# Performance work log

Hardware: AMD Instinct MI355X
Metric: run time of the kernel (lower is better)

The kernel has to match this reference:

```python
import jax, jax.numpy as jnp
import numpy as np


def _knn_idx(query, ref, k):
    # query [B,Q,F], ref [B,M,F] -> indices [B,Q,k] of k nearest refs (L2)
    d2 = (jnp.sum(query * query, -1)[..., None]
          - 2.0 * jnp.einsum('bqf,bmf->bqm', query, ref)
          + jnp.sum(ref * ref, -1)[:, None, :])
    _, idx = jax.lax.top_k(-d2, k)
    return idx


def _gather(pts, idx):
    # pts [B,M,F], idx [B,Q,k] -> [B,Q,k,F]
    return jax.vmap(lambda p, i: p[i])(pts, idx)


def _mlp(h, W1, b1, W2, b2):
    # pointwise 1x1-conv MLP: Conv1d(k=1) == per-point matmul
    return jax.nn.relu(h @ W1 + b1) @ W2 + b2


def setup_inputs() -> dict:
    key = jax.random.key(0)
    ks = jax.random.split(key, 12)
    B, N, S1, S2 = 8, 16384, 512, 128

    def p(k, shape, fan):
        return jax.random.normal(k, shape, jnp.float32) / np.float32(np.sqrt(fan))

    return {
        'x': jax.random.normal(ks[0], (B, N, 3), jnp.float32),
        'sample_idx1': jnp.sort(jax.random.randint(ks[1], (S1,), 0, N)),
        'sample_idx2': jnp.sort(jax.random.randint(ks[2], (S2,), 0, S1)),
        'sa1_W1': p(ks[3], (3, 64), 3), 'sa1_b1': jnp.zeros((64,), jnp.float32),
        'sa1_W2': p(ks[4], (64, 64), 64), 'sa1_b2': jnp.zeros((64,), jnp.float32),
        'sa2_W1': p(ks[5], (64, 128), 64), 'sa2_b1': jnp.zeros((128,), jnp.float32),
        'sa2_W2': p(ks[6], (128, 128), 128), 'sa2_b2': jnp.zeros((128,), jnp.float32),
        'fp1_W1': p(ks[7], (192, 64), 192), 'fp1_b1': jnp.zeros((64,), jnp.float32),
        'fp1_W2': p(ks[8], (64, 64), 64), 'fp1_b2': jnp.zeros((64,), jnp.float32),
        'fp2_W1': p(ks[9], (67, 32), 67), 'fp2_b1': jnp.zeros((32,), jnp.float32),
        'fp2_W2': p(ks[10], (32, 32), 32), 'fp2_b2': jnp.zeros((32,), jnp.float32),
        'fc_W': p(ks[11], (32, 2), 32), 'fc_b': jnp.zeros((2,), jnp.float32),
    }


def reference(x, sample_idx1, sample_idx2,
              sa1_W1, sa1_b1, sa1_W2, sa1_b2,
              sa2_W1, sa2_b1, sa2_W2, sa2_b2,
              fp1_W1, fp1_b1, fp1_W2, fp1_b2,
              fp2_W1, fp2_b1, fp2_W2, fp2_b2,
              fc_W, fc_b):
    G = 32  # group_points
    # --- SetAbstraction 1 (KNN grouping in xyz space) ---
    samp1 = x[:, sample_idx1]                                  # [B,S1,3]
    g1 = _gather(x, _knn_idx(samp1, x, G))                     # [B,S1,G,3]
    feat1 = jnp.max(_mlp(g1, sa1_W1, sa1_b1, sa1_W2, sa1_b2), axis=2)   # [B,S1,64]
    # --- SetAbstraction 2 (point cloud = SA1 features, as in source) ---
    samp2 = feat1[:, sample_idx2]                              # [B,S2,64]
    g2 = _gather(feat1, _knn_idx(samp2, feat1, G))             # [B,S2,G,64]
    feat2 = jnp.max(_mlp(g2, sa2_W1, sa2_b1, sa2_W2, sa2_b2), axis=2)   # [B,S2,128]
    coords2 = samp1[:, sample_idx2]                            # [B,S2,3]
    # --- FeaturePropagation 1: interpolate feat2 onto the S1 points (3-NN mean) ---
    interp1 = jnp.mean(_gather(feat2, _knn_idx(samp1, coords2, 3)), axis=2)  # [B,S1,128]
    h1 = _mlp(jnp.concatenate([feat1, interp1], -1), fp1_W1, fp1_b1, fp1_W2, fp1_b2)  # [B,S1,64]
    # --- FeaturePropagation 2: interpolate onto all N points ---
    interp2 = jnp.mean(_gather(h1, _knn_idx(x, samp1, 3)), axis=2)           # [B,N,64]
    h2 = _mlp(jnp.concatenate([x, interp2], -1), fp2_W1, fp2_b1, fp2_W2, fp2_b2)      # [B,N,32]
    return jax.nn.sigmoid(h2 @ fc_W + fc_b)                    # [B,N,2]
```

## Files before the change

### kernel.cpp

```cpp
#include <hip/hip_runtime.h>
#include <hip/hip_bf16.h>

#define NB   8
#define NPTS 16384
#define NS1  512
#define NS2  128
#define KNN  32
#define FINF 3.402823466e+38f

__device__ __forceinline__ unsigned sortkey(float f) {
  unsigned u = __float_as_uint(f);
  unsigned m = (u & 0x80000000u) ? 0xFFFFFFFFu : 0x80000000u;
  return u ^ m;
}

__device__ __forceinline__ void topk32_round(unsigned long long key, int lane,
                                             unsigned long long& lkey,
                                             unsigned long long& tau) {
  unsigned long long mask = __ballot(key < tau);
  while (mask) {
    int src = __ffsll(mask) - 1;
    mask &= mask - 1;
    unsigned long long cand = __shfl(key, src);
    if (cand < tau) {
      unsigned long long up = __shfl_up(lkey, 1);
      if (lane == 0) up = 0ull;
      unsigned long long nk = (lkey < cand) ? lkey : (up < cand ? cand : up);
      if (lane < 32) lkey = nk;
      tau = __shfl(lkey, 31);
    }
  }
}

__device__ __forceinline__ void merge3(float& d0, int& j0, float& d1, int& j1,
                                       float& d2, int& j2, int xm) {
  float e0 = __shfl_xor(d0, xm), e1 = __shfl_xor(d1, xm), e2 = __shfl_xor(d2, xm);
  int   f0 = __shfl_xor(j0, xm), f1 = __shfl_xor(j1, xm), f2 = __shfl_xor(j2, xm);
  float a0 = d0, a1 = d1, a2 = d2;
  int   b0 = j0, b1 = j1, b2 = j2;
  float od0, od1, od2; int oj0, oj1, oj2;
  #pragma unroll
  for (int r = 0; r < 3; ++r) {
    bool ta = (a0 < e0) || (a0 == e0 && b0 < f0);
    float sd = ta ? a0 : e0; int sj = ta ? b0 : f0;
    a0 = ta ? a1 : a0;  b0 = ta ? b1 : b0;
    a1 = ta ? a2 : a1;  b1 = ta ? b2 : b1;
    a2 = ta ? FINF : a2;
    e0 = ta ? e0 : e1;  f0 = ta ? f0 : f1;
    e1 = ta ? e1 : e2;  f1 = ta ? f1 : f2;
    e2 = ta ? e2 : FINF;
    if (r == 0) { od0 = sd; oj0 = sj; }
    else if (r == 1) { od1 = sd; oj1 = sj; }
    else { od2 = sd; oj2 = sj; }
  }
  d0 = od0; j0 = oj0; d1 = od1; j1 = oj1; d2 = od2; j2 = oj2;
}

extern "C" __global__ void __launch_bounds__(256)
prep_kernel(const float* __restrict__ x, float4* __restrict__ xr) {
  const int i = blockIdx.x * 256 + threadIdx.x;
  const float rx = x[i*3+0], ry = x[i*3+1], rz = x[i*3+2];
  xr[i] = make_float4(rx, ry, rz, rx*rx + ry*ry + rz*rz);
}

extern "C" __global__ void __launch_bounds__(256)
knn1_kernel(const float4* __restrict__ xr, const int* __restrict__ sidx1,
            int* __restrict__ idx1) {
  const int w = threadIdx.x >> 6, lane = threadIdx.x & 63;
  const int gq = blockIdx.x * 4 + w;
  const int b = gq >> 9, q = gq & (NS1 - 1);
  const float4* xb = xr + (size_t)b * NPTS;
  const float4 Q = xb[sidx1[q]];
  unsigned long long lkey = ~0ull, tau = ~0ull;
  float4 r = xb[lane];
  for (int t = 0; t < NPTS/64; ++t) {
    float4 rn = r;
    if (t < NPTS/64 - 1) rn = xb[(t+1)*64 + lane];
    const float d = (Q.w - 2.0f*(Q.x*r.x + Q.y*r.y + Q.z*r.z)) + r.w;
    const unsigned long long key =
        ((unsigned long long)sortkey(d) << 32) | (unsigned)(t*64 + lane);
    unsigned long long mask = __ballot(key < tau);
    while (mask) {
      const int src = (int)(__ffsll((long long)mask) - 1);
      mask &= mask - 1;
      const unsigned clo = (unsigned)__builtin_amdgcn_readlane((int)(unsigned)key, src);
      const unsigned chi = (unsigned)__builtin_amdgcn_readlane((int)(unsigned)(key >> 32), src);
      const unsigned long long cand = ((unsigned long long)chi << 32) | clo;
      if (cand < tau) {
        unsigned long long up = __shfl_up(lkey, 1);
        if (lane == 0) up = 0ull;
        unsigned long long nk = (lkey < cand) ? lkey : (up < cand ? cand : up);
        if (lane < 32) lkey = nk;
        const unsigned tlo = (unsigned)__builtin_amdgcn_readlane((int)(unsigned)lkey, 31);
        const unsigned thi = (unsigned)__builtin_amdgcn_readlane((int)(unsigned)(lkey >> 32), 31);
        tau = ((unsigned long long)thi << 32) | tlo;
      }
    }
    r = rn;
  }
  if (lane < 32) idx1[gq*KNN + lane] = (int)(unsigned)lkey;
}

extern "C" __global__ void __launch_bounds__(256)
mlp1_kernel(const float* __restrict__ x, const int* __restrict__ sidx1,
            const int* __restrict__ idx1,
            const float* __restrict__ W1, const float* __restrict__ b1,
            const float* __restrict__ W2, const float* __restrict__ b2,
            float* __restrict__ feat1, float* __restrict__ rr1,
            float* __restrict__ samp1) {
  __shared__ float P[32][3];
  __shared__ float H[32][64];
  __shared__ float PM[4][64];
  const int tid = threadIdx.x;
  const int gq = blockIdx.x;
  const int b = gq >> 9, q = gq & (NS1-1);
  const float* xb = x + (size_t)b * NPTS * 3;
  const int* nb = idx1 + gq * KNN;
  if (tid < 96) { int n = tid/3, d = tid - n*3; P[n][d] = xb[nb[n]*3 + d]; }
  __syncthreads();
  #pragma unroll
  for (int i = 0; i < 8; ++i) {
    int e = tid + 256*i, n = e >> 6, c = e & 63;
    float h = b1[c] + P[n][0]*W1[c] + P[n][1]*W1[64+c] + P[n][2]*W1[128+c];
    H[n][c] = fmaxf(h, 0.0f);
  }
  __syncthreads();
  const int g = tid >> 6, c = tid & 63;
  float acc[8];
  #pragma unroll
  for (int k = 0; k < 8; ++k) acc[k] = 0.0f;
  for (int j = 0; j < 64; j += 4) {
    float w0 = W2[j*64+c], w1 = W2[(j+1)*64+c], w2 = W2[(j+2)*64+c], w3 = W2[(j+3)*64+c];
    #pragma unroll
    for (int k = 0; k < 8; ++k) {
      float4 h4 = *(const float4*)&H[g*8+k][j];
      acc[k] = fmaf(h4.w, w3, fmaf(h4.z, w2, fmaf(h4.y, w1, fmaf(h4.x, w0, acc[k]))));
    }
  }
  float m = acc[0];
  #pragma unroll
  for (int k = 1; k < 8; ++k) m = fmaxf(m, acc[k]);
  PM[g][c] = m;
  __syncthreads();
  if (tid < 64) {
    float v = fmaxf(fmaxf(PM[0][tid], PM[1][tid]), fmaxf(PM[2][tid], PM[3][tid])) + b2[tid];
    feat1[(size_t)gq*64 + tid] = v;
    float s = v*v;
    #pragma unroll
    for (int off = 32; off; off >>= 1) s += __shfl_xor(s, off);
    if (tid == 0) rr1[gq] = s;
  } else if (tid < 67) {
    int d = tid - 64;
    samp1[(size_t)gq*3 + d] = xb[sidx1[q]*3 + d];
  }
}

extern "C" __global__ void __launch_bounds__(256)
knn2_kernel(const float* __restrict__ feat1, const float* __restrict__ rr1,
            const int* __restrict__ sidx2, int* __restrict__ idx2) {
  __shared__ float qrow[4][64];
  const int w = threadIdx.x >> 6, lane = threadIdx.x & 63;
  const int gq = blockIdx.x*4 + w;
  const int b = gq >> 7, q = gq & (NS2-1);
  const int sq = sidx2[q];
  const float* f1b = feat1 + (size_t)b * NS1 * 64;
  const float* rrb = rr1 + b * NS1;
  qrow[w][lane] = f1b[sq*64 + lane];
  __syncthreads();
  const float qq = rrb[sq];
  unsigned long long lkey = ~0ull, tau = ~0ull;
  for (int t = 0; t < NS1/64; ++t) {
    const int j = t*64 + lane;
    const float* rrow = f1b + j*64;
    float dot = 0.0f;
    #pragma unroll
    for (int f = 0; f < 64; f += 4) {
      float4 r4 = *(const float4*)(rrow + f);
      dot = fmaf(qrow[w][f+3], r4.w, fmaf(qrow[w][f+2], r4.z,
            fmaf(qrow[w][f+1], r4.y, fmaf(qrow[w][f+0], r4.x, dot))));
    }
    const float d = (qq - 2.0f*dot) + rrb[j];
    const unsigned long long key =
        ((unsigned long long)sortkey(d) << 32) | (unsigned)j;
    topk32_round(key, lane, lkey, tau);
  }
  if (lane < 32) idx2[gq*KNN + lane] = (int)(unsigned)lkey;
}

extern "C" __global__ void __launch_bounds__(256)
mlp2_kernel(const float* __restrict__ feat1, const int* __restrict__ idx2,
            const float* __restrict__ W1, const float* __restrict__ b1,
            const float* __restrict__ W2, const float* __restrict__ b2,
            float* __restrict__ feat2) {
  __shared__ float Gm[32][64];
  __shared__ float H[32][128];
  __shared__ float PM[2][128];
  const int tid = threadIdx.x;
  const int gq = blockIdx.x;
  const int b = gq >> 7;
  const float* f1b = feat1 + (size_t)b * NS1 * 64;
  const int* nb = idx2 + gq * KNN;
  #pragma unroll
  for (int i = 0; i < 8; ++i) {
    int e = tid + 256*i, n = e >> 6, f = e & 63;
    Gm[n][f] = f1b[nb[n]*64 + f];
  }
  __syncthreads();
  #pragma unroll
  for (int i = 0; i < 16; ++i) {
    int e = tid + 256*i, n = e >> 7, c = e & 127;
    float h = b1[c];
    for (int f = 0; f < 64; f += 4) {
      float4 g4 = *(const float4*)&Gm[n][f];
      h = fmaf(g4.x, W1[f*128+c], h);
      h = fmaf(g4.y, W1[(f+1)*128+c], h);
      h = fmaf(g4.z, W1[(f+2)*128+c], h);
      h = fmaf(g4.w, W1[(f+3)*128+c], h);
    }
    H[n][c] = fmaxf(h, 0.0f);
  }
  __syncthreads();
  const int g = tid >> 7, c = tid & 127;
  float acc[16];
  #pragma unroll
  for (int k = 0; k < 16; ++k) acc[k] = 0.0f;
  for (int j = 0; j < 128; j += 4) {
    float w0 = W2[j*128+c], w1 = W2[(j+1)*128+c], w2 = W2[(j+2)*128+c], w3 = W2[(j+3)*128+c];
    #pragma unroll
    for (int k = 0; k < 16; ++k) {
      float4 h4 = *(const float4*)&H[g*16+k][j];
      acc[k] = fmaf(h4.w, w3, fmaf(h4.z, w2, fmaf(h4.y, w1, fmaf(h4.x, w0, acc[k]))));
    }
  }
  float m = acc[0];
  #pragma unroll
  for (int k = 1; k < 16; ++k) m = fmaxf(m, acc[k]);
  PM[g][c] = m;
  __syncthreads();
  if (tid < 128) feat2[(size_t)gq*128 + tid] = fmaxf(PM[0][tid], PM[1][tid]) + b2[tid];
}

extern "C" __global__ void __launch_bounds__(256)
fp1_kernel(const float* __restrict__ samp1, const int* __restrict__ sidx2,
           const float* __restrict__ feat1, const float* __restrict__ feat2,
           const float* __restrict__ W1, const float* __restrict__ b1,
           const float* __restrict__ W2, const float* __restrict__ b2,
           float* __restrict__ h1) {
  __shared__ float interp[4][128];
  __shared__ float hbuf[4][64];
  const int w = threadIdx.x >> 6, lane = threadIdx.x & 63;
  const int gq = blockIdx.x*4 + w;
  const int b = gq >> 9, q = gq & (NS1-1);
  const float* s1b = samp1 + (size_t)b * NS1 * 3;
  const float qx = s1b[q*3+0], qy = s1b[q*3+1], qz = s1b[q*3+2];
  const float qq = qx*qx + qy*qy + qz*qz;
  float d0, d1; int j0i, j1i;
  {
    const int rs = sidx2[lane];
    const float rx = s1b[rs*3+0], ry = s1b[rs*3+1], rz = s1b[rs*3+2];
    d0 = (qq - 2.0f*(qx*rx+qy*ry+qz*rz)) + (rx*rx+ry*ry+rz*rz);
    j0i = lane;
  }
  {
    const int j = lane + 64;
    const int rs = sidx2[j];
    const float rx = s1b[rs*3+0], ry = s1b[rs*3+1], rz = s1b[rs*3+2];
    d1 = (qq - 2.0f*(qx*rx+qy*ry+qz*rz)) + (rx*rx+ry*ry+rz*rz);
    j1i = j;
  }
  if (d1 < d0) { float td = d0; d0 = d1; d1 = td; int tj = j0i; j0i = j1i; j1i = tj; }
  float dA = d0, dB = d1, dC = FINF;
  int   jA = j0i, jB = j1i, jC = 0;
  merge3(dA, jA, dB, jB, dC, jC, 1);
  merge3(dA, jA, dB, jB, dC, jC, 2);
  merge3(dA, jA, dB, jB, dC, jC, 4);
  merge3(dA, jA, dB, jB, dC, jC, 8);
  merge3(dA, jA, dB, jB, dC, jC, 16);
  merge3(dA, jA, dB, jB, dC, jC, 32);
  const int r0 = jA, r1 = jB, r2 = jC;
  const float* f2b = feat2 + (size_t)b * NS2 * 128;
  interp[w][lane] =
      (f2b[r0*128+lane] + f2b[r1*128+lane] + f2b[r2*128+lane]) * (1.0f/3.0f);
  interp[w][lane+64] =
      (f2b[r0*128+64+lane] + f2b[r1*128+64+lane] + f2b[r2*128+64+lane]) * (1.0f/3.0f);
  __syncthreads();
  const float* f1row = feat1 + (size_t)gq * 64;
  float h = b1[lane];
  for (int f = 0; f < 64; ++f)  h = fmaf(f1row[f], W1[f*64+lane], h);
  for (int f = 0; f < 128; ++f) h = fmaf(interp[w][f], W1[(64+f)*64+lane], h);
  hbuf[w][lane] = fmaxf(h, 0.0f);
  __syncthreads();
  float o = b2[lane];
  for (int f = 0; f < 64; ++f) o = fmaf(hbuf[w][f], W2[f*64+lane], o);
  h1[(size_t)gq*64 + lane] = o;
}

extern "C" __global__ void __launch_bounds__(256, 4)
fp2a_kernel(const float* __restrict__ x, const float* __restrict__ samp1,
            ushort4* __restrict__ knn3) {
  __shared__ float4 RS[NS1];
  const int tid = threadIdx.x;
  const int b = blockIdx.x >> 8;
  const int pbase = (blockIdx.x & 255) * 64;
  for (int e = tid; e < NS1; e += 256) {
    const float rx = samp1[((size_t)b*NS1 + e)*3 + 0];
    const float ry = samp1[((size_t)b*NS1 + e)*3 + 1];
    const float rz = samp1[((size_t)b*NS1 + e)*3 + 2];
    RS[e] = make_float4(rx, ry, rz, rx*rx + ry*ry + rz*rz);
  }
  __syncthreads();
  const int p = pbase + (tid >> 2);
  const int q4 = tid & 3;
  const float* xb = x + (size_t)b * NPTS * 3;
  const float qx = xb[p*3+0], qy = xb[p*3+1], qz = xb[p*3+2];
  const float qq = qx*qx + qy*qy + qz*qz;
  float d0 = FINF, d1 = FINF, d2 = FINF;
  int j0 = 0, j1 = 0, j2 = 0;
  const float4* RQ = RS + q4*128;
  #pragma unroll 4
  for (int i = 0; i < 128; ++i) {
    const float4 r = RQ[i];
    const float dot = qx*r.x + qy*r.y + qz*r.z;
    const float d = (qq - 2.0f*dot) + r.w;
    const int j = q4*128 + i;
    const bool c2 = d < d2, c1 = d < d1, c0 = d < d0;
    d2 = c1 ? d1 : (c2 ? d : d2);  j2 = c1 ? j1 : (c2 ? j : j2);
    d1 = c0 ? d0 : (c1 ? d : d1);  j1 = c0 ? j0 : (c1 ? j : j1);
    d0 = c0 ? d : d0;              j0 = c0 ? j : j0;
  }
  merge3(d0, j0, d1, j1, d2, j2, 1);
  merge3(d0, j0, d1, j1, d2, j2, 2);
  if (q4 == 0) {
    ushort4 o;
    o.x = (unsigned short)j0; o.y = (unsigned short)j1;
    o.z = (unsigned short)j2; o.w = 0;
    knn3[(size_t)b*NPTS + p] = o;
  }
}

extern "C" __global__ void __launch_bounds__(256, 4)
fp2b_kernel(const float* __restrict__ x, const ushort4* __restrict__ knn3,
            const float* __restrict__ h1,
            const float* __restrict__ W1, const float* __restrict__ b1,
            const float* __restrict__ W2, const float* __restrict__ b2,
            const float* __restrict__ fcW, const float* __restrict__ fcb,
            float* __restrict__ out) {
  __shared__ float Xe[64][68];
  __shared__ float W1s[67*32];
  __shared__ float Hs[64][36];
  __shared__ ushort4 kid[64];
  __shared__ float WcS[64];
  __shared__ float bcS[2];
  const int tid = threadIdx.x;
  const int b = blockIdx.x >> 8;
  const int pbase = (blockIdx.x & 255) * 64;
  const float* xb = x + (size_t)b * NPTS * 3;
  const float* h1b = h1 + (size_t)b * NS1 * 64;
  if (tid < 64) {
    kid[tid] = knn3[(size_t)b*NPTS + pbase + tid];
    Xe[tid][0] = xb[(pbase+tid)*3+0];
    Xe[tid][1] = xb[(pbase+tid)*3+1];
    Xe[tid][2] = xb[(pbase+tid)*3+2];
  }
  for (int e = tid; e < 67*32; e += 256) W1s[e] = W1[e];
  __syncthreads();
  {
    const int sub = tid >> 6, f = tid & 63;
    #pragma unroll 4
    for (int i = 0; i < 16; ++i) {
      const int p = i*4 + sub;
      const ushort4 kk = kid[p];
      const float v = (h1b[(int)kk.x*64 + f] + h1b[(int)kk.y*64 + f] +
                       h1b[(int)kk.z*64 + f]) * (1.0f/3.0f);
      Xe[p][3+f] = v;
    }
  }
  __syncthreads();
  if (tid < 64) {
    const int k = tid >> 1, col = tid & 1;
    float s = 0.0f;
    for (int c = 0; c < 32; ++c) s = fmaf(W2[k*32+c], fcW[c*2+col], s);
    WcS[k*2+col] = s;
  } else if (tid < 66) {
    const int col = tid & 1;
    float s = fcb[col];
    for (int c = 0; c < 32; ++c) s = fmaf(b2[c], fcW[c*2+col], s);
    bcS[col] = s;
  }
  {
    const int p = tid >> 2, c0 = (tid & 3) * 8;
    float acc[8];
    const float4 bb0 = *(const float4*)(b1 + c0);
    const float4 bb1 = *(const float4*)(b1 + c0 + 4);
    acc[0]=bb0.x; acc[1]=bb0.y; acc[2]=bb0.z; acc[3]=bb0.w;
    acc[4]=bb1.x; acc[5]=bb1.y; acc[6]=bb1.z; acc[7]=bb1.w;
    for (int f = 0; f < 67; ++f) {
      const float xv = Xe[p][f];
      const float4 w0 = *(const float4*)&W1s[f*32 + c0];
      const float4 w1 = *(const float4*)&W1s[f*32 + c0 + 4];
      acc[0] = fmaf(xv, w0.x, acc[0]);
      acc[1] = fmaf(xv, w0.y, acc[1]);
      acc[2] = fmaf(xv, w0.z, acc[2]);
      acc[3] = fmaf(xv, w0.w, acc[3]);
      acc[4] = fmaf(xv, w1.x, acc[4]);
      acc[5] = fmaf(xv, w1.y, acc[5]);
      acc[6] = fmaf(xv, w1.z, acc[6]);
      acc[7] = fmaf(xv, w1.w, acc[7]);
    }
    *(float4*)&Hs[p][c0]   = make_float4(fmaxf(acc[0],0.f), fmaxf(acc[1],0.f),
                                         fmaxf(acc[2],0.f), fmaxf(acc[3],0.f));
    *(float4*)&Hs[p][c0+4] = make_float4(fmaxf(acc[4],0.f), fmaxf(acc[5],0.f),
                                         fmaxf(acc[6],0.f), fmaxf(acc[7],0.f));
  }
  __syncthreads();
  if (tid < 128) {
    const int p = tid >> 1, col = tid & 1;
    float s = bcS[col];
    for (int c = 0; c < 32; ++c) s = fmaf(Hs[p][c], WcS[c*2+col], s);
    out[((size_t)b*NPTS + pbase + p)*2 + col] = 1.0f / (1.0f + expf(-s));
  }
}

extern "C" void kernel_launch(void* const* d_in, const int* in_sizes, int n_in,
                              void* d_out, int out_size, void* d_ws, size_t ws_size,
                              hipStream_t stream) {
  const float* x     = (const float*)d_in[0];
  const int*   sidx1 = (const int*)d_in[1];
  const int*   sidx2 = (const int*)d_in[2];
  const float* sa1W1 = (const float*)d_in[3];
  const float* sa1b1 = (const float*)d_in[4];
  const float* sa1W2 = (const float*)d_in[5];
  const float* sa1b2 = (const float*)d_in[6];
  const float* sa2W1 = (const float*)d_in[7];
  const float* sa2b1 = (const float*)d_in[8];
  const float* sa2W2 = (const float*)d_in[9];
  const float* sa2b2 = (const float*)d_in[10];
  const float* fp1W1 = (const float*)d_in[11];
  const float* fp1b1 = (const float*)d_in[12];
  const float* fp1W2 = (const float*)d_in[13];
  const float* fp1b2 = (const float*)d_in[14];
  const float* fp2W1 = (const float*)d_in[15];
  const float* fp2b1 = (const float*)d_in[16];
  const float* fp2W2 = (const float*)d_in[17];
  const float* fp2b2 = (const float*)d_in[18];
  const float* fcW   = (const float*)d_in[19];
  const float* fcb   = (const float*)d_in[20];
  float* out = (float*)d_out;

  char* ws = (char*)d_ws;
  float4* xr   = (float4*)(ws + 0);
  float* feat1 = (float*)(ws + 0);
  float* rr1   = (float*)(ws + 1048576);
  float* samp1 = (float*)(ws + 1064960);
  float* feat2 = (float*)(ws + 1114112);
  float* h1    = (float*)(ws + 1638400);
  int*   idx1  = (int*)  (ws + 2686976);
  int*   idx2  = (int*)  (ws + 3211264);
  ushort4* knn3 = (ushort4*)(ws + 0);

  hipLaunchKernelGGL(prep_kernel, dim3(512), dim3(256), 0, stream, x, xr);
  hipLaunchKernelGGL(knn1_kernel, dim3(1024), dim3(256), 0, stream,
                     xr, sidx1, idx1);
  hipLaunchKernelGGL(mlp1_kernel, dim3(4096), dim3(256), 0, stream,
                     x, sidx1, idx1, sa1W1, sa1b1, sa1W2, sa1b2,
                     feat1, rr1, samp1);
  hipLaunchKernelGGL(knn2_kernel, dim3(256), dim3(256), 0, stream,
                     feat1, rr1, sidx2, idx2);
  hipLaunchKernelGGL(mlp2_kernel, dim3(1024), dim3(256), 0, stream,
                     feat1, idx2, sa2W1, sa2b1, sa2W2, sa2b2, feat2);
  hipLaunchKernelGGL(fp1_kernel, dim3(1024), dim3(256), 0, stream,
                     samp1, sidx2, feat1, feat2, fp1W1, fp1b1, fp1W2, fp1b2, h1);
  hipLaunchKernelGGL(fp2a_kernel, dim3(2048), dim3(256), 0, stream,
                     x, samp1, knn3);
  hipLaunchKernelGGL(fp2b_kernel, dim3(2048), dim3(256), 0, stream,
                     x, knn3, h1, fp2W1, fp2b1, fp2W2, fp2b2, fcW, fcb, out);
}
```

Before: 282.2 us.

## Split KNN1 scan across two waves with 32-bit keys and DPP insertion

```diff
diff --git a/kernel.cpp b/kernel.cpp
--- a/kernel.cpp
+++ b/kernel.cpp
@@ -14,20 +14,29 @@
   return u ^ m;
 }
 
-__device__ __forceinline__ void topk32_round(unsigned long long key, int lane,
-                                             unsigned long long& lkey,
-                                             unsigned long long& tau) {
+__device__ __forceinline__ void topk32_u32(unsigned key, int idx, int lane,
+                                           unsigned& lkey, int& lidx,
+                                           unsigned& tau) {
+  const bool is16 = (lane == 16);
   unsigned long long mask = __ballot(key < tau);
   while (mask) {
-    int src = __ffsll(mask) - 1;
+    const int src = (int)(__ffsll((long long)mask) - 1);
     mask &= mask - 1;
-    unsigned long long cand = __shfl(key, src);
-    if (cand < tau) {
-      unsigned long long up = __shfl_up(lkey, 1);
-      if (lane == 0) up = 0ull;
-      unsigned long long nk = (lkey < cand) ? lkey : (up < cand ? cand : up);
-      if (lane < 32) lkey = nk;
-      tau = __shfl(lkey, 31);
+    const unsigned ck = (unsigned)__builtin_amdgcn_readlane((int)key, src);
+    if (ck < tau) {
+      const int ci = __builtin_amdgcn_readlane(idx, src);
+      const int upk0 = __builtin_amdgcn_update_dpp(0, (int)lkey, 0x111, 0xf, 0xf, true);
+      const int upi0 = __builtin_amdgcn_update_dpp(0, lidx, 0x111, 0xf, 0xf, true);
+      const int pk = __builtin_amdgcn_readlane((int)lkey, 15);
+      const int pi = __builtin_amdgcn_readlane(lidx, 15);
+      const unsigned up  = is16 ? (unsigned)pk : (unsigned)upk0;
+      const int     upi  = is16 ? pi : upi0;
+      const bool keep  = (lkey <= ck);
+      const bool useup = (up > ck);
+      const unsigned nk = keep ? lkey : (useup ? up : ck);
+      const int     ni  = keep ? lidx : (useup ? upi : ci);
+      if (lane < 32) { lkey = nk; lidx = ni; }
+      tau = (unsigned)__builtin_amdgcn_readlane((int)lkey, 31);
     }
   }
 }
@@ -63,42 +72,47 @@
   xr[i] = make_float4(rx, ry, rz, rx*rx + ry*ry + rz*rz);
 }
 
-extern "C" __global__ void __launch_bounds__(256)
+#define PROC32(rr, jbase)                                                     \
+  {                                                                           \
+    const float d = (Q.w - 2.0f*(Q.x*rr.x + Q.y*rr.y + Q.z*rr.z)) + rr.w;     \
+    topk32_u32(sortkey(d), (jbase) + lane, lane, lkey, lidx, tau);            \
+  }
+
+extern "C" __global__ void __launch_bounds__(256, 8)
 knn1_kernel(const float4* __restrict__ xr, const int* __restrict__ sidx1,
             int* __restrict__ idx1) {
+  __shared__ unsigned SK[2][32];
+  __shared__ int      SI[2][32];
   const int w = threadIdx.x >> 6, lane = threadIdx.x & 63;
-  const int gq = blockIdx.x * 4 + w;
+  const int lq = w >> 1, half = w & 1;
+  const int gq = blockIdx.x * 2 + lq;
   const int b = gq >> 9, q = gq & (NS1 - 1);
   const float4* xb = xr + (size_t)b * NPTS;
   const float4 Q = xb[sidx1[q]];
-  unsigned long long lkey = ~0ull, tau = ~0ull;
-  float4 r = xb[lane];
-  for (int t = 0; t < NPTS/64; ++t) {
-    float4 rn = r;
-    if (t < NPTS/64 - 1) rn = xb[(t+1)*64 + lane];
-    const float d = (Q.w - 2.0f*(Q.x*r.x + Q.y*r.y + Q.z*r.z)) + r.w;
-    const unsigned long long key =
-        ((unsigned long long)sortkey(d) << 32) | (unsigned)(t*64 + lane);
-    unsigned long long mask = __ballot(key < tau);
-    while (mask) {
-      const int src = (int)(__ffsll((long long)mask) - 1);
-      mask &= mask - 1;
-      const unsigned clo = (unsigned)__builtin_amdgcn_readlane((int)(unsigned)key, src);
-      const unsigned chi = (unsigned)__builtin_amdgcn_readlane((int)(unsigned)(key >> 32), src);
-      const unsigned long long cand = ((unsigned long long)chi << 32) | clo;
-      if (cand < tau) {
-        unsigned long long up = __shfl_up(lkey, 1);
-        if (lane == 0) up = 0ull;
-        unsigned long long nk = (lkey < cand) ? lkey : (up < cand ? cand : up);
-        if (lane < 32) lkey = nk;
-        const unsigned tlo = (unsigned)__builtin_amdgcn_readlane((int)(unsigned)lkey, 31);
-        const unsigned thi = (unsigned)__builtin_amdgcn_readlane((int)(unsigned)(lkey >> 32), 31);
-        tau = ((unsigned long long)thi << 32) | tlo;
-      }
-    }
-    r = rn;
-  }
-  if (lane < 32) idx1[gq*KNN + lane] = (int)(unsigned)lkey;
+  const float4* xw = xb + half * (NPTS/2);
+  const int jb0 = half * (NPTS/2);
+  unsigned lkey = 0xFFFFFFFFu, tau = 0xFFFFFFFFu;
+  int lidx = 0;
+  float4 r0 = xw[0*64+lane], r1 = xw[1*64+lane], r2 = xw[2*64+lane], r3 = xw[3*64+lane];
+  float4 r4 = xw[4*64+lane], r5 = xw[5*64+lane], r6 = xw[6*64+lane], r7 = xw[7*64+lane];
+  for (int t = 0; t < 128; t += 8) {
+    PROC32(r0, jb0 + (t+0)*64);  r0 = xw[((t+ 8)&127)*64 + lane];
+    PROC32(r1, jb0 + (t+1)*64);  r1 = xw[((t+ 9)&127)*64 + lane];
+    PROC32(r2, jb0 + (t+2)*64);  r2 = xw[((t+10)&127)*64 + lane];
+    PROC32(r3, jb0 + (t+3)*64);  r3 = xw[((t+11)&127)*64 + lane];
+    PROC32(r4, jb0 + (t+4)*64);  r4 = xw[((t+12)&127)*64 + lane];
+    PROC32(r5, jb0 + (t+5)*64);  r5 = xw[((t+13)&127)*64 + lane];
+    PROC32(r6, jb0 + (t+6)*64);  r6 = xw[((t+14)&127)*64 + lane];
+    PROC32(r7, jb0 + (t+7)*64);  r7 = xw[((t+15)&127)*64 + lane];
+  }
+  if (half == 1 && lane < 32) { SK[lq][lane] = lkey; SI[lq][lane] = lidx; }
+  __syncthreads();
+  if (half == 0) {
+    const unsigned mk = (lane < 32) ? SK[lq][lane] : 0xFFFFFFFFu;
+    const int      mi = (lane < 32) ? SI[lq][lane] : 0;
+    topk32_u32(mk, mi, lane, lkey, lidx, tau);
+    if (lane < 32) idx1[gq*KNN + lane] = lidx;
+  }
 }
 
 extern "C" __global__ void __launch_bounds__(256)
@@ -168,7 +182,8 @@
   qrow[w][lane] = f1b[sq*64 + lane];
   __syncthreads();
   const float qq = rrb[sq];
-  unsigned long long lkey = ~0ull, tau = ~0ull;
+  unsigned lkey = 0xFFFFFFFFu, tau = 0xFFFFFFFFu;
+  int lidx = 0;
   for (int t = 0; t < NS1/64; ++t) {
     const int j = t*64 + lane;
     const float* rrow = f1b + j*64;
@@ -180,11 +195,9 @@
             fmaf(qrow[w][f+1], r4.y, fmaf(qrow[w][f+0], r4.x, dot))));
     }
     const float d = (qq - 2.0f*dot) + rrb[j];
-    const unsigned long long key =
-        ((unsigned long long)sortkey(d) << 32) | (unsigned)j;
-    topk32_round(key, lane, lkey, tau);
-  }
-  if (lane < 32) idx2[gq*KNN + lane] = (int)(unsigned)lkey;
+    topk32_u32(sortkey(d), j, lane, lkey, lidx, tau);
+  }
+  if (lane < 32) idx2[gq*KNN + lane] = lidx;
 }
 
 extern "C" __global__ void __launch_bounds__(256)
@@ -459,7 +472,7 @@
   ushort4* knn3 = (ushort4*)(ws + 0);
 
   hipLaunchKernelGGL(prep_kernel, dim3(512), dim3(256), 0, stream, x, xr);
-  hipLaunchKernelGGL(knn1_kernel, dim3(1024), dim3(256), 0, stream,
+  hipLaunchKernelGGL(knn1_kernel, dim3(2048), dim3(256), 0, stream,
                      xr, sidx1, idx1);
   hipLaunchKernelGGL(mlp1_kernel, dim3(4096), dim3(256), 0, stream,
                      x, sidx1, idx1, sa1W1, sa1b1, sa1W2, sa1b2,
```

After: 273.4 us. 3.1% less time.
